# Optimization experiments

Measured on AMD Instinct MI355X. Metric: run time of the kernel, lower is better.

Reference implementation:

```python
import jax, jax.numpy as jnp
import numpy as np

NF = 64          # num_features
DG = 8           # deform_groups (== weight groups == offset groups)
KK = 9           # 3x3 kernel taps
OFF_CH = DG * 2 * KK   # 144 offset channels
MSK_CH = DG * KK       # 72 mask channels


def conv3x3(x, w):
    # x: [B,C,H,W], w: [O,I,3,3], stride 1, pad 1, no bias
    return jax.lax.conv_general_dilated(
        x, w, window_strides=(1, 1), padding=((1, 1), (1, 1)),
        dimension_numbers=('NCHW', 'OIHW', 'NCHW'))


def deform_conv(x, offset, mask, w, b):
    """Modulated deformable conv (torchvision DeformConv2d semantics).
    x: [B,C,H,W]; offset: [B,2*DG*KK,H,W] (per group/tap (dy,dx) pairs);
    mask: [B,DG*KK,H,W] (already sigmoid'ed); w: [C, C//DG, 3, 3]; b: [C].
    """
    B, C, H, W = x.shape
    Cg = C // DG
    off = offset.reshape(B, DG, KK, 2, H, W)
    dy, dx = off[:, :, :, 0], off[:, :, :, 1]          # [B,G,K,H,W]
    ky = (jnp.arange(KK) // 3 - 1).astype(x.dtype).reshape(1, 1, KK, 1, 1)
    kx = (jnp.arange(KK) % 3 - 1).astype(x.dtype).reshape(1, 1, KK, 1, 1)
    py = dy + ky + jnp.arange(H, dtype=x.dtype).reshape(1, 1, 1, H, 1)
    px = dx + kx + jnp.arange(W, dtype=x.dtype).reshape(1, 1, 1, 1, W)

    xf = x.reshape(B, DG, Cg, H * W)
    y0 = jnp.floor(py)
    x0 = jnp.floor(px)
    ly = py - y0
    lx = px - x0

    acc = jnp.zeros((B, DG, Cg, KK * H * W), dtype=x.dtype)
    for yy, wy in ((y0, 1.0 - ly), (y0 + 1.0, ly)):
        for xx, wx in ((x0, 1.0 - lx), (x0 + 1.0, lx)):
            valid = (yy >= 0) & (yy < H) & (xx >= 0) & (xx < W)
            yi = jnp.clip(yy, 0, H - 1).astype(jnp.int32)
            xi = jnp.clip(xx, 0, W - 1).astype(jnp.int32)
            idx = (yi * W + xi).reshape(B, DG, KK * H * W)
            v = jnp.take_along_axis(xf, idx[:, :, None, :], axis=3)  # [B,G,Cg,KHW]
            wgt = jnp.where(valid, wy * wx, 0.0).reshape(B, DG, 1, KK * H * W)
            acc = acc + v * wgt

    sampled = acc.reshape(B, DG, Cg, KK, H * W)
    sampled = sampled * mask.reshape(B, DG, 1, KK, H * W)
    wg = w.reshape(DG, C // DG, Cg, KK)                 # [G, Og, Cg, K]
    out = jnp.einsum('gock,bgckn->bgon', wg, sampled)   # [B,G,Og,HW]
    return out.reshape(B, C, H, W) + b.reshape(1, C, 1, 1)


def offset_gen(o):
    # chunk into 3 along channels: offset = cat(o1,o2) = first 144 ch, mask = sigmoid(last 72)
    return o[:, :OFF_CH], jax.nn.sigmoid(o[:, OFF_CH:])


def setup_inputs() -> dict:
    key = jax.random.key(0)
    ks = jax.random.split(key, 16)
    s = 0.05
    inp = {
        'burst_feat': jax.random.normal(ks[0], (1, 8, NF, 96, 96), jnp.float32),
        'bottleneck_w': jax.random.normal(ks[1], (NF, 2 * NF, 3, 3), jnp.float32) * s,
    }
    for i in range(4):
        inp[f'off_w{i+1}'] = jax.random.normal(ks[2 + i], (OFF_CH + MSK_CH, NF, 3, 3), jnp.float32) * s
        inp[f'def_w{i+1}'] = jax.random.normal(ks[6 + i], (NF, NF // DG, 3, 3), jnp.float32) * s
        inp[f'def_b{i+1}'] = jax.random.normal(ks[10 + i], (NF,), jnp.float32) * s
    return inp


def reference(burst_feat, bottleneck_w,
              off_w1, off_w2, off_w3, off_w4,
              def_w1, def_w2, def_w3, def_w4,
              def_b1, def_b2, def_b3, def_b4):
    B, N, F, H, W = burst_feat.shape
    ref = jnp.broadcast_to(burst_feat[:, 0:1], (B, N, F, H, W))
    feat = jnp.concatenate([burst_feat, ref], axis=2).reshape(B * N, 2 * F, H, W)
    feat = conv3x3(feat, bottleneck_w)
    for ow, dw, db in ((off_w1, def_w1, def_b1), (off_w2, def_w2, def_b2),
                       (off_w3, def_w3, def_b3), (off_w4, def_w4, def_b4)):
        offset, mask = offset_gen(conv3x3(feat, ow))
        feat = deform_conv(feat, offset, mask, dw, db)
    return feat.reshape(B, N, F, H, W)
```

## Files before the change

### kernel.cpp

```cpp
#include <hip/hip_runtime.h>
#include <math.h>

#define HW    9216
#define HDIM  96
#define WDIM  96
#define NIMG  8
#define CF    64
#define OFFCH 144
#define MSKCH 72
#define OMC   216
#define NT    36
#define LSTR  44

typedef unsigned short u16;
typedef unsigned int   u32;
typedef _Float16 f16;
typedef __attribute__((ext_vector_type(8))) _Float16 f16x8;
typedef __attribute__((ext_vector_type(4))) float f32x4;
typedef __attribute__((ext_vector_type(4))) u32 u32x4;

__device__ inline u16 f16b(f16 h){ u16 r; __builtin_memcpy(&r, &h, 2); return r; }
__device__ inline f16 b16f(u16 b){ f16 h; __builtin_memcpy(&h, &b, 2); return h; }

__global__ void pack_w_k(const float* __restrict__ bw,
                         const float* __restrict__ ow0, const float* __restrict__ ow1,
                         const float* __restrict__ ow2, const float* __restrict__ ow3,
                         const float* __restrict__ dw0, const float* __restrict__ dw1,
                         const float* __restrict__ dw2, const float* __restrict__ dw3,
                         u16* __restrict__ wp, float* __restrict__ dwp)
{
    const float* ows[4] = {ow0, ow1, ow2, ow3};
    const float* dws[4] = {dw0, dw1, dw2, dw3};
    int total = 73728 + 4 * 124416;
    for (int j = blockIdx.x * blockDim.x + threadIdx.x; j < total;
         j += gridDim.x * blockDim.x) {
        if (j < 73728) {
            int oc = j / 1152, r = j % 1152, ci = r / 9, tap = r % 9;
            wp[(size_t)(oc * 9 + tap) * 128 + ci] = f16b((f16)bw[j]);
        } else {
            int k = j - 73728;
            int layer = k / 124416, r = k % 124416;
            int oc = r / 576, r3 = r % 576, ci = r3 / 9, tap = r3 % 9;
            wp[73728 + (size_t)layer * 129024 + (size_t)(oc * 9 + tap) * 64 + ci] =
                f16b((f16)ows[layer][r]);
        }
    }
    for (int j = blockIdx.x * blockDim.x + threadIdx.x; j < 4 * 4608;
         j += gridDim.x * blockDim.x) {
        int layer = j / 4608, e = j % 4608;
        wp[73728 + (size_t)layer * 129024 + 124416 + e] = 0;
    }
    for (int j = blockIdx.x * blockDim.x + threadIdx.x; j < 4 * 8 * 576;
         j += gridDim.x * blockDim.x) {
        int layer = j / 4608, r = j % 4608, g = r / 576, e = r % 576;
        int kk = e / 64, c = (e / 8) % 8, o = e % 8;
        dwp[j] = dws[layer][(size_t)(g * 8 + o) * 72 + c * 9 + kk];
    }
}

__global__ __launch_bounds__(256) void prep_cat_k(
    const float* __restrict__ burst, u16* __restrict__ cat)
{
    __shared__ float tb[32 * 257];
    const int id = blockIdx.x;
    const int n = id & 7, tile = id >> 3;
    const int oy = (tile / 6) * 16, ox = (tile % 6) * 16;
    const int tid = threadIdx.x;

    for (int pass = 0; pass < 4; ++pass) {
        const float* src = (pass < 2) ? burst + (size_t)n * CF * HW : burst;
        const int chb = (pass & 1) * 32;
        __syncthreads();
        {
            int c = tid >> 3, q = tid & 7;
            const float* sp = src + (size_t)(chb + c) * HW;
#pragma unroll
            for (int rr = 0; rr < 2; ++rr) {
                int row = q * 2 + rr;
                const float* rp = sp + (oy + row) * WDIM + ox;
#pragma unroll
                for (int jj = 0; jj < 4; ++jj) {
                    f32x4 v = *(const f32x4*)(rp + jj * 4);
                    int px = row * 16 + jj * 4;
                    tb[c * 257 + px + 0] = v.x;
                    tb[c * 257 + px + 1] = v.y;
                    tb[c * 257 + px + 2] = v.z;
                    tb[c * 257 + px + 3] = v.w;
                }
            }
        }
        __syncthreads();
        {
            int p = tid;
#pragma unroll
            for (int cq = 0; cq < 4; ++cq) {
                u32 wd[4];
#pragma unroll
                for (int e = 0; e < 4; ++e) {
                    int c0 = cq * 8 + e * 2;
                    u16 h0 = f16b((f16)tb[c0 * 257 + p]);
                    u16 h1 = f16b((f16)tb[(c0 + 1) * 257 + p]);
                    wd[e] = (u32)h0 | ((u32)h1 << 16);
                }
                u32x4 hv = {wd[0], wd[1], wd[2], wd[3]};
                int plane = pass * 4 + cq;
                *(u32x4*)(cat + ((size_t)((n * NT + tile) * 16 + plane) * 256 + p) * 8) = hv;
            }
        }
    }
}

template<int PLANES, int MODE>
__global__ __launch_bounds__(256, 4) void conv_mfma_k(
    const u16* __restrict__ inb,
    const u16* __restrict__ w_hi,
    u16* __restrict__ om_out,
    u16* __restrict__ out_feat)
{
    __shared__ __align__(16) u16 lds[324 * LSTR];

    const int CIN = PLANES * 8;
    const int id = blockIdx.x;
    const int n = id & 7, w = id >> 3;
    const int tile = (MODE == 0) ? (w >> 1) : (w / 7);
    const int ocg  = (MODE == 0) ? (w & 1)  : (w % 7);
    const int tid = threadIdx.x;
    const int wv = tid >> 6, lane = tid & 63;
    const int lx = lane & 15, lg = lane >> 4;
    const int oy = (tile / 6) * 16, ox = (tile % 6) * 16;

    f32x4 acc1[2][4];
#pragma unroll
    for (int t = 0; t < 2; ++t)
#pragma unroll
        for (int r = 0; r < 4; ++r)
            acc1[t][r] = (f32x4){0.f, 0.f, 0.f, 0.f};

    const u16* inb_n = inb + (size_t)(n * NT) * PLANES * 2048;
    const u16* wr0 = w_hi + (size_t)((ocg * 32 + lx) * 9) * CIN + lg * 8;
    const u16* wr1 = w_hi + (size_t)((ocg * 32 + 16 + lx) * 9) * CIN + lg * 8;

    for (int chk = 0; chk < PLANES / 4; ++chk) {
        __syncthreads();
        for (int u = tid; u < 1296; u += 256) {
            int pos = u >> 2, q = u & 3;
            int yy = pos / 18, xx = pos - yy * 18;
            int gy = oy + yy - 1, gx = ox + xx - 1;
            u32x4 val = {0u, 0u, 0u, 0u};
            if (gy >= 0 && gy < HDIM && gx >= 0 && gx < WDIM) {
                int tof = (gy >> 4) * 6 + (gx >> 4);
                int pin = (gy & 15) * 16 + (gx & 15);
                val = *(const u32x4*)(inb_n +
                    ((size_t)(tof * PLANES + chk * 4 + q) * 256 + pin) * 8);
            }
            *(u32x4*)(lds + pos * LSTR + q * 8) = val;
        }
        __syncthreads();

        const u16* wc0 = wr0 + chk * 32;
        const u16* wc1 = wr1 + chk * 32;
        const u16* lbase = lds + (wv * 4) * 18 * LSTR + lx * LSTR + lg * 8;

        f16x8 aw0 = *(const f16x8*)(wc0);
        f16x8 aw1 = *(const f16x8*)(wc1);
        f16x8 bfr[4];
#pragma unroll
        for (int r = 0; r < 4; ++r)
            bfr[r] = *(const f16x8*)(lbase + r * 18 * LSTR);

#pragma unroll
        for (int tap = 0; tap < 9; ++tap) {
            f16x8 na0, na1, nb[4];
            if (tap < 8) {
                const int ntap = tap + 1;
                const int nky = ntap / 3, nkx = ntap - nky * 3;
                na0 = *(const f16x8*)(wc0 + (size_t)ntap * CIN);
                na1 = *(const f16x8*)(wc1 + (size_t)ntap * CIN);
#pragma unroll
                for (int r = 0; r < 4; ++r)
                    nb[r] = *(const f16x8*)(lbase + ((r + nky) * 18 + nkx) * LSTR);
            }
#pragma unroll
            for (int r = 0; r < 4; ++r) {
                acc1[0][r] = __builtin_amdgcn_mfma_f32_16x16x32_f16(aw0, bfr[r], acc1[0][r], 0, 0, 0);
                acc1[1][r] = __builtin_amdgcn_mfma_f32_16x16x32_f16(aw1, bfr[r], acc1[1][r], 0, 0, 0);
            }
            if (tap < 8) {
                aw0 = na0; aw1 = na1;
#pragma unroll
                for (int r = 0; r < 4; ++r) bfr[r] = nb[r];
            }
        }
    }

    if (MODE == 0) {
        __syncthreads();
        u16* tb = lds;
#pragma unroll
        for (int t = 0; t < 2; ++t)
#pragma unroll
            for (int r = 0; r < 4; ++r) {
                int px = (wv * 4 + r) * 16 + lx;
#pragma unroll
                for (int v = 0; v < 4; ++v)
                    tb[px * LSTR + t * 16 + lg * 4 + v] = f16b((f16)acc1[t][r][v]);
            }
        __syncthreads();
        const int p = tid;
        const u16* srcr = tb + p * LSTR;
#pragma unroll
        for (int cq = 0; cq < 4; ++cq) {
            *(u32x4*)(out_feat + ((size_t)((n * NT + tile) * 8 + ocg * 4 + cq) * 256 + p) * 8)
                = *(const u32x4*)(srcr + cq * 8);
        }
    } else {
        __syncthreads();
        u16* tb = lds;
#pragma unroll
        for (int t = 0; t < 2; ++t) {
            const bool sig = (ocg * 32 + t * 16) >= OFFCH;
#pragma unroll
            for (int r = 0; r < 4; ++r) {
                int px = (wv * 4 + r) * 16 + lx;
#pragma unroll
                for (int v = 0; v < 4; ++v) {
                    float val = acc1[t][r][v];
                    if (sig) val = 1.f / (1.f + __expf(-val));
                    tb[(t * 16 + lg * 4 + v) * 264 + px] = f16b((f16)val);
                }
            }
        }
        __syncthreads();
        const int ocl = tid >> 3, q = tid & 7;
        const int ch = ocg * 32 + ocl;
        if (ch < OMC) {
            u16* dst = om_out + ((size_t)(n * NT + tile) * OMC + ch) * 256;
            const u16* srcr = tb + ocl * 264;
#pragma unroll
            for (int j = 0; j < 4; ++j) {
                int un = (q + j * 8) * 8;
                *(u32x4*)(dst + un) = *(const u32x4*)(srcr + un);
            }
        }
    }
}

template<int LAST>
__global__ __launch_bounds__(256, 4) void deform_k(
    const u16* __restrict__ feat,
    const u16* __restrict__ om,
    const float* __restrict__ wgtp, const float* __restrict__ bias,
    u16* __restrict__ out_feat, float* __restrict__ out32)
{
    const int id = blockIdx.x;
    const int n = id & 7, w = id >> 3;
    const int tile = w >> 3, g = w & 7;

    const int ty = threadIdx.x >> 4, tx = threadIdx.x & 15;
    const int h  = (tile / 6) * 16 + ty;
    const int wx = (tile % 6) * 16 + tx;
    const int pix = h * WDIM + wx;
    const int pixT = ty * 16 + tx;

    const float* wg = wgtp + (size_t)g * 576;
    const u16* ob = om + (size_t)(n * NT + tile) * OMC * 256;
    const u16* fbase = feat + (size_t)(n * NT) * 8 * 2048 + g * 2048;

    float acc[8];
#pragma unroll
    for (int o = 0; o < 8; ++o) acc[o] = 0.f;

#pragma unroll
    for (int k = 0; k < 9; ++k) {
        float dy = (float)b16f(ob[(g * 18 + 2 * k    ) * 256 + pixT]);
        float dx = (float)b16f(ob[(g * 18 + 2 * k + 1) * 256 + pixT]);
        float m  = (float)b16f(ob[(OFFCH + g * 9 + k) * 256 + pixT]);

        float py = dy + (float)(k / 3 - 1) + (float)h;
        float px = dx + (float)(k % 3 - 1) + (float)wx;
        float y0f = floorf(py), x0f = floorf(px);
        float ly = py - y0f, lx = px - x0f;
        int y0 = (int)y0f, x0 = (int)x0f;
        int y1 = y0 + 1,   x1 = x0 + 1;

        bool vy0 = (y0 >= 0) && (y0 < HDIM);
        bool vy1 = (y1 >= 0) && (y1 < HDIM);
        bool vx0 = (x0 >= 0) && (x0 < WDIM);
        bool vx1 = (x1 >= 0) && (x1 < WDIM);

        float w00 = (vy0 && vx0) ? (1.f - ly) * (1.f - lx) : 0.f;
        float w01 = (vy0 && vx1) ? (1.f - ly) * lx         : 0.f;
        float w10 = (vy1 && vx0) ? ly * (1.f - lx)         : 0.f;
        float w11 = (vy1 && vx1) ? ly * lx                 : 0.f;

        int y0c = min(max(y0, 0), HDIM - 1), y1c = min(max(y1, 0), HDIM - 1);
        int x0c = min(max(x0, 0), WDIM - 1), x1c = min(max(x1, 0), WDIM - 1);

        auto ga = [&](int y, int x) -> const f16x8* {
            int tof = (y >> 4) * 6 + (x >> 4);
            int pin = (y & 15) * 16 + (x & 15);
            return (const f16x8*)(fbase + (size_t)tof * 16384 + pin * 8);
        };
        f16x8 C00 = *ga(y0c, x0c);
        f16x8 C01 = *ga(y0c, x1c);
        f16x8 C10 = *ga(y1c, x0c);
        f16x8 C11 = *ga(y1c, x1c);

#pragma unroll
        for (int c = 0; c < 8; ++c) {
            float v =      w00 * (float)C00[c];
            v = fmaf(w01, (float)C01[c], v);
            v = fmaf(w10, (float)C10[c], v);
            v = fmaf(w11, (float)C11[c], v);
            v *= m;
            const float* w8 = wg + (k * 8 + c) * 8;
#pragma unroll
            for (int o = 0; o < 8; ++o)
                acc[o] = fmaf(w8[o], v, acc[o]);
        }
    }

    if (LAST) {
#pragma unroll
        for (int o = 0; o < 8; ++o)
            out32[((size_t)n * CF + g * 8 + o) * HW + pix] = acc[o] + bias[g * 8 + o];
    } else {
        u16 hb[8];
#pragma unroll
        for (int o = 0; o < 8; ++o)
            hb[o] = f16b((f16)(acc[o] + bias[g * 8 + o]));
        u32x4 hv;
        hv.x = (u32)hb[0] | ((u32)hb[1] << 16); hv.y = (u32)hb[2] | ((u32)hb[3] << 16);
        hv.z = (u32)hb[4] | ((u32)hb[5] << 16); hv.w = (u32)hb[6] | ((u32)hb[7] << 16);
        *(u32x4*)(out_feat + ((size_t)((n * NT + tile) * 8 + g) * 256 + pixT) * 8) = hv;
    }
}

extern "C" void kernel_launch(void* const* d_in, const int* in_sizes, int n_in,
                              void* d_out, int out_size, void* d_ws, size_t ws_size,
                              hipStream_t stream) {
    const float* burst = (const float*)d_in[0];
    const float* bw    = (const float*)d_in[1];

    const float* ow[4]; const float* dw[4]; const float* db[4];
    bool interleaved = (in_sizes[3] == 64 * 8 * 9);
    for (int i = 0; i < 4; ++i) {
        if (interleaved) {
            ow[i] = (const float*)d_in[2 + 3 * i];
            dw[i] = (const float*)d_in[3 + 3 * i];
            db[i] = (const float*)d_in[4 + 3 * i];
        } else {
            ow[i] = (const float*)d_in[2 + i];
            dw[i] = (const float*)d_in[6 + i];
            db[i] = (const float*)d_in[10 + i];
        }
    }

    float* out = (float*)d_out;

    u16*   om    = (u16*)d_ws;
    u16*   featB = om + 15925248;
    u16*   wp    = featB + 4718592;
    float* dwp   = (float*)(wp + 589824);
    u16*   cat   = (u16*)d_ws;
    u16*   featA = (u16*)d_out;

    const u16* wp_b = wp;
    const u16* wp_o[4];
    for (int i = 0; i < 4; ++i)
        wp_o[i] = wp + 73728 + (size_t)i * 129024;

    pack_w_k<<<dim3(512), dim3(256), 0, stream>>>(
        bw, ow[0], ow[1], ow[2], ow[3], dw[0], dw[1], dw[2], dw[3], wp, dwp);
    prep_cat_k<<<dim3(288), dim3(256), 0, stream>>>(burst, cat);

    conv_mfma_k<16, 0><<<dim3(576), dim3(256), 0, stream>>>(
        cat, wp_b, nullptr, featA);

    u16* fx = featA;
    u16* fy = featB;
    for (int i = 0; i < 4; ++i) {
        conv_mfma_k<8, 1><<<dim3(2016), dim3(256), 0, stream>>>(
            fx, wp_o[i], om, nullptr);
        if (i < 3) {
            deform_k<0><<<dim3(2304), dim3(256), 0, stream>>>(
                fx, om, dwp + (size_t)i * 4608, db[i], fy, nullptr);
            u16* t = fx; fx = fy; fy = t;
        } else {
            deform_k<1><<<dim3(2304), dim3(256), 0, stream>>>(
                fx, om, dwp + (size_t)i * 4608, db[i], nullptr, out);
        }
    }
}
```

Before: 385.5 us.

## Widen offset-conv tiles to 16x32 so each weight fragment feeds two pixel tiles

The offset/mask convolution kernel gains a TX template parameter. With TX=2 each block covers two horizontally adjacent 16x16 tiles: it stages a wider halo in LDS and reuses every weight fragment across both tiles, which halves the grid and the global weight loads. The cost is doubled accumulator registers and a larger LDS footprint, so launch bounds drop to 3 blocks per CU. The epilogue writes both tiles, and the LDS row stride changes to 40 for the wide path.

```diff
diff --git a/kernel.cpp b/kernel.cpp
--- a/kernel.cpp
+++ b/kernel.cpp
@@ -10,7 +10,6 @@
 #define MSKCH 72
 #define OMC   216
 #define NT    36
-#define LSTR  44
 
 typedef unsigned short u16;
 typedef unsigned int   u32;
@@ -110,31 +109,44 @@
     }
 }
 
-template<int PLANES, int MODE>
-__global__ __launch_bounds__(256, 4) void conv_mfma_k(
+template<int PLANES, int MODE, int TX>
+__global__ __launch_bounds__(256, 3) void conv_mfma_k(
     const u16* __restrict__ inb,
     const u16* __restrict__ w_hi,
     u16* __restrict__ om_out,
     u16* __restrict__ out_feat)
 {
-    __shared__ __align__(16) u16 lds[324 * LSTR];
-
-    const int CIN = PLANES * 8;
+    constexpr int CIN   = PLANES * 8;
+    constexpr int HALOW = 16 * TX + 2;
+    constexpr int HSTR  = (TX == 2) ? 40 : 44;
+    constexpr int POSN  = 18 * HALOW;
+    __shared__ __align__(16) u16 lds[POSN * HSTR];
+
     const int id = blockIdx.x;
     const int n = id & 7, w = id >> 3;
-    const int tile = (MODE == 0) ? (w >> 1) : (w / 7);
-    const int ocg  = (MODE == 0) ? (w & 1)  : (w % 7);
+    int tile0, ocg, oy, ox;
+    if (TX == 1) {
+        tile0 = (MODE == 0) ? (w >> 1) : (w / 7);
+        ocg   = (MODE == 0) ? (w & 1)  : (w % 7);
+        oy = (tile0 / 6) * 16; ox = (tile0 % 6) * 16;
+    } else {
+        int region = w / 7; ocg = w % 7;
+        int trow = region / 3, tp = region % 3;
+        tile0 = trow * 6 + tp * 2;
+        oy = trow * 16; ox = tp * 32;
+    }
     const int tid = threadIdx.x;
     const int wv = tid >> 6, lane = tid & 63;
     const int lx = lane & 15, lg = lane >> 4;
-    const int oy = (tile / 6) * 16, ox = (tile % 6) * 16;
-
-    f32x4 acc1[2][4];
+
+    f32x4 acc[2][4][TX];
 #pragma unroll
     for (int t = 0; t < 2; ++t)
 #pragma unroll
         for (int r = 0; r < 4; ++r)
-            acc1[t][r] = (f32x4){0.f, 0.f, 0.f, 0.f};
+#pragma unroll
+            for (int s = 0; s < TX; ++s)
+                acc[t][r][s] = (f32x4){0.f, 0.f, 0.f, 0.f};
 
     const u16* inb_n = inb + (size_t)(n * NT) * PLANES * 2048;
     const u16* wr0 = w_hi + (size_t)((ocg * 32 + lx) * 9) * CIN + lg * 8;
@@ -142,9 +154,9 @@
 
     for (int chk = 0; chk < PLANES / 4; ++chk) {
         __syncthreads();
-        for (int u = tid; u < 1296; u += 256) {
+        for (int u = tid; u < POSN * 4; u += 256) {
             int pos = u >> 2, q = u & 3;
-            int yy = pos / 18, xx = pos - yy * 18;
+            int yy = pos / HALOW, xx = pos - yy * HALOW;
             int gy = oy + yy - 1, gx = ox + xx - 1;
             u32x4 val = {0u, 0u, 0u, 0u};
             if (gy >= 0 && gy < HDIM && gx >= 0 && gx < WDIM) {
@@ -153,42 +165,70 @@
                 val = *(const u32x4*)(inb_n +
                     ((size_t)(tof * PLANES + chk * 4 + q) * 256 + pin) * 8);
             }
-            *(u32x4*)(lds + pos * LSTR + q * 8) = val;
+            *(u32x4*)(lds + pos * HSTR + q * 8) = val;
         }
         __syncthreads();
 
         const u16* wc0 = wr0 + chk * 32;
         const u16* wc1 = wr1 + chk * 32;
-        const u16* lbase = lds + (wv * 4) * 18 * LSTR + lx * LSTR + lg * 8;
-
-        f16x8 aw0 = *(const f16x8*)(wc0);
-        f16x8 aw1 = *(const f16x8*)(wc1);
-        f16x8 bfr[4];
-#pragma unroll
-        for (int r = 0; r < 4; ++r)
-            bfr[r] = *(const f16x8*)(lbase + r * 18 * LSTR);
-
-#pragma unroll
-        for (int tap = 0; tap < 9; ++tap) {
-            f16x8 na0, na1, nb[4];
-            if (tap < 8) {
-                const int ntap = tap + 1;
-                const int nky = ntap / 3, nkx = ntap - nky * 3;
-                na0 = *(const f16x8*)(wc0 + (size_t)ntap * CIN);
-                na1 = *(const f16x8*)(wc1 + (size_t)ntap * CIN);
+
+        if (TX == 1) {
+            const u16* lbase = lds + (wv * 4) * HALOW * HSTR + lx * HSTR + lg * 8;
+            f16x8 aw0 = *(const f16x8*)(wc0);
+            f16x8 aw1 = *(const f16x8*)(wc1);
+            f16x8 bfr[4];
+#pragma unroll
+            for (int r = 0; r < 4; ++r)
+                bfr[r] = *(const f16x8*)(lbase + r * HALOW * HSTR);
+#pragma unroll
+            for (int tap = 0; tap < 9; ++tap) {
+                f16x8 na0, na1, nb[4];
+                if (tap < 8) {
+                    const int ntap = tap + 1;
+                    const int nky = ntap / 3, nkx = ntap - nky * 3;
+                    na0 = *(const f16x8*)(wc0 + (size_t)ntap * CIN);
+                    na1 = *(const f16x8*)(wc1 + (size_t)ntap * CIN);
+#pragma unroll
+                    for (int r = 0; r < 4; ++r)
+                        nb[r] = *(const f16x8*)(lbase + ((r + nky) * HALOW + nkx) * HSTR);
+                }
+#pragma unroll
+                for (int r = 0; r < 4; ++r) {
+                    acc[0][r][0] = __builtin_amdgcn_mfma_f32_16x16x32_f16(aw0, bfr[r], acc[0][r][0], 0, 0, 0);
+                    acc[1][r][0] = __builtin_amdgcn_mfma_f32_16x16x32_f16(aw1, bfr[r], acc[1][r][0], 0, 0, 0);
+                }
+                if (tap < 8) {
+                    aw0 = na0; aw1 = na1;
+#pragma unroll
+                    for (int r = 0; r < 4; ++r) bfr[r] = nb[r];
+                }
+            }
+        } else {
+            f16x8 aw0 = *(const f16x8*)(wc0);
+            f16x8 aw1 = *(const f16x8*)(wc1);
+#pragma unroll
+            for (int tap = 0; tap < 9; ++tap) {
+                f16x8 na0, na1;
+                if (tap < 8) {
+                    na0 = *(const f16x8*)(wc0 + (size_t)(tap + 1) * CIN);
+                    na1 = *(const f16x8*)(wc1 + (size_t)(tap + 1) * CIN);
+                }
+                const int ky = tap / 3, kx = tap - ky * 3;
+                f16x8 bfr[4][2];
 #pragma unroll
                 for (int r = 0; r < 4; ++r)
-                    nb[r] = *(const f16x8*)(lbase + ((r + nky) * 18 + nkx) * LSTR);
-            }
-#pragma unroll
-            for (int r = 0; r < 4; ++r) {
-                acc1[0][r] = __builtin_amdgcn_mfma_f32_16x16x32_f16(aw0, bfr[r], acc1[0][r], 0, 0, 0);
-                acc1[1][r] = __builtin_amdgcn_mfma_f32_16x16x32_f16(aw1, bfr[r], acc1[1][r], 0, 0, 0);
-            }
-            if (tap < 8) {
-                aw0 = na0; aw1 = na1;
-#pragma unroll
-                for (int r = 0; r < 4; ++r) bfr[r] = nb[r];
+#pragma unroll
+                    for (int s = 0; s < 2; ++s)
+                        bfr[r][s] = *(const f16x8*)(lds +
+                            ((size_t)((wv * 4 + r + ky) * HALOW + s * 16 + lx + kx)) * HSTR + lg * 8);
+#pragma unroll
+                for (int r = 0; r < 4; ++r)
+#pragma unroll
+                    for (int s = 0; s < 2; ++s) {
+                        acc[0][r][s] = __builtin_amdgcn_mfma_f32_16x16x32_f16(aw0, bfr[r][s], acc[0][r][s], 0, 0, 0);
+                        acc[1][r][s] = __builtin_amdgcn_mfma_f32_16x16x32_f16(aw1, bfr[r][s], acc[1][r][s], 0, 0, 0);
+                    }
+                if (tap < 8) { aw0 = na0; aw1 = na1; }
             }
         }
     }
@@ -203,14 +243,14 @@
                 int px = (wv * 4 + r) * 16 + lx;
 #pragma unroll
                 for (int v = 0; v < 4; ++v)
-                    tb[px * LSTR + t * 16 + lg * 4 + v] = f16b((f16)acc1[t][r][v]);
+                    tb[px * HSTR + t * 16 + lg * 4 + v] = f16b((f16)acc[t][r][0][v]);
             }
         __syncthreads();
         const int p = tid;
-        const u16* srcr = tb + p * LSTR;
+        const u16* srcr = tb + p * HSTR;
 #pragma unroll
         for (int cq = 0; cq < 4; ++cq) {
-            *(u32x4*)(out_feat + ((size_t)((n * NT + tile) * 8 + ocg * 4 + cq) * 256 + p) * 8)
+            *(u32x4*)(out_feat + ((size_t)((n * NT + tile0) * 8 + ocg * 4 + cq) * 256 + p) * 8)
                 = *(const u32x4*)(srcr + cq * 8);
         }
     } else {
@@ -221,25 +261,30 @@
             const bool sig = (ocg * 32 + t * 16) >= OFFCH;
 #pragma unroll
             for (int r = 0; r < 4; ++r) {
-                int px = (wv * 4 + r) * 16 + lx;
-#pragma unroll
-                for (int v = 0; v < 4; ++v) {
-                    float val = acc1[t][r][v];
-                    if (sig) val = 1.f / (1.f + __expf(-val));
-                    tb[(t * 16 + lg * 4 + v) * 264 + px] = f16b((f16)val);
-                }
+                int rowpx = (wv * 4 + r) * 16 + lx;
+#pragma unroll
+                for (int s = 0; s < 2; ++s)
+#pragma unroll
+                    for (int v = 0; v < 4; ++v) {
+                        float val = acc[t][r][s][v];
+                        if (sig) val = 1.f / (1.f + __expf(-val));
+                        tb[(t * 16 + lg * 4 + v) * 514 + s * 256 + rowpx] = f16b((f16)val);
+                    }
             }
         }
         __syncthreads();
         const int ocl = tid >> 3, q = tid & 7;
         const int ch = ocg * 32 + ocl;
         if (ch < OMC) {
-            u16* dst = om_out + ((size_t)(n * NT + tile) * OMC + ch) * 256;
-            const u16* srcr = tb + ocl * 264;
-#pragma unroll
-            for (int j = 0; j < 4; ++j) {
-                int un = (q + j * 8) * 8;
-                *(u32x4*)(dst + un) = *(const u32x4*)(srcr + un);
+            const u16* srcr = tb + ocl * 514;
+#pragma unroll
+            for (int s = 0; s < 2; ++s) {
+                u16* dst = om_out + ((size_t)(n * NT + tile0 + s) * OMC + ch) * 256;
+#pragma unroll
+                for (int j = 0; j < 4; ++j) {
+                    int un = (q + j * 8) * 8;
+                    *(u32x4*)(dst + un) = *(const u32x4*)(srcr + s * 256 + un);
+                }
             }
         }
     }
@@ -374,13 +419,13 @@
         bw, ow[0], ow[1], ow[2], ow[3], dw[0], dw[1], dw[2], dw[3], wp, dwp);
     prep_cat_k<<<dim3(288), dim3(256), 0, stream>>>(burst, cat);
 
-    conv_mfma_k<16, 0><<<dim3(576), dim3(256), 0, stream>>>(
+    conv_mfma_k<16, 0, 1><<<dim3(576), dim3(256), 0, stream>>>(
         cat, wp_b, nullptr, featA);
 
     u16* fx = featA;
     u16* fy = featB;
     for (int i = 0; i < 4; ++i) {
-        conv_mfma_k<8, 1><<<dim3(2016), dim3(256), 0, stream>>>(
+        conv_mfma_k<8, 1, 2><<<dim3(1008), dim3(256), 0, stream>>>(
             fx, wp_o[i], om, nullptr);
         if (i < 3) {
             deform_k<0><<<dim3(2304), dim3(256), 0, stream>>>(
```

Result: no change. 387.9 us (+0.6%).

## Split conv tile across eight waves and load B fragments per tap

Applied to the files above, without the earlier changes.

The MFMA conv kernel now runs 512 threads (8 waves) per block. Each wave covers 2 row-blocks of the 16x16 tile instead of 4, which halves the per-wave accumulators. The B-fragment software prefetch is dropped in favour of loading LDS fragments at each tap, and the store epilogues are redistributed across the larger block. The aim is lower register pressure and more waves in flight to hide latency, at the cost of less per-wave reuse of the weight fragments and less LDS-load/MFMA overlap.

```diff
diff --git a/kernel.cpp b/kernel.cpp
--- a/kernel.cpp
+++ b/kernel.cpp
@@ -111,7 +111,7 @@
 }
 
 template<int PLANES, int MODE>
-__global__ __launch_bounds__(256, 4) void conv_mfma_k(
+__global__ __launch_bounds__(512, 6) void conv_mfma_k(
     const u16* __restrict__ inb,
     const u16* __restrict__ w_hi,
     u16* __restrict__ om_out,
@@ -129,12 +129,12 @@
     const int lx = lane & 15, lg = lane >> 4;
     const int oy = (tile / 6) * 16, ox = (tile % 6) * 16;
 
-    f32x4 acc1[2][4];
+    f32x4 acc[2][2];
 #pragma unroll
     for (int t = 0; t < 2; ++t)
 #pragma unroll
-        for (int r = 0; r < 4; ++r)
-            acc1[t][r] = (f32x4){0.f, 0.f, 0.f, 0.f};
+        for (int r = 0; r < 2; ++r)
+            acc[t][r] = (f32x4){0.f, 0.f, 0.f, 0.f};
 
     const u16* inb_n = inb + (size_t)(n * NT) * PLANES * 2048;
     const u16* wr0 = w_hi + (size_t)((ocg * 32 + lx) * 9) * CIN + lg * 8;
@@ -142,7 +142,7 @@
 
     for (int chk = 0; chk < PLANES / 4; ++chk) {
         __syncthreads();
-        for (int u = tid; u < 1296; u += 256) {
+        for (int u = tid; u < 1296; u += 512) {
             int pos = u >> 2, q = u & 3;
             int yy = pos / 18, xx = pos - yy * 18;
             int gy = oy + yy - 1, gx = ox + xx - 1;
@@ -159,37 +159,29 @@
 
         const u16* wc0 = wr0 + chk * 32;
         const u16* wc1 = wr1 + chk * 32;
-        const u16* lbase = lds + (wv * 4) * 18 * LSTR + lx * LSTR + lg * 8;
+        const u16* lbase = lds + (wv * 2) * 18 * LSTR + lx * LSTR + lg * 8;
 
         f16x8 aw0 = *(const f16x8*)(wc0);
         f16x8 aw1 = *(const f16x8*)(wc1);
-        f16x8 bfr[4];
-#pragma unroll
-        for (int r = 0; r < 4; ++r)
-            bfr[r] = *(const f16x8*)(lbase + r * 18 * LSTR);
 
 #pragma unroll
         for (int tap = 0; tap < 9; ++tap) {
-            f16x8 na0, na1, nb[4];
+            f16x8 na0, na1;
             if (tap < 8) {
-                const int ntap = tap + 1;
-                const int nky = ntap / 3, nkx = ntap - nky * 3;
-                na0 = *(const f16x8*)(wc0 + (size_t)ntap * CIN);
-                na1 = *(const f16x8*)(wc1 + (size_t)ntap * CIN);
-#pragma unroll
-                for (int r = 0; r < 4; ++r)
-                    nb[r] = *(const f16x8*)(lbase + ((r + nky) * 18 + nkx) * LSTR);
-            }
-#pragma unroll
-            for (int r = 0; r < 4; ++r) {
-                acc1[0][r] = __builtin_amdgcn_mfma_f32_16x16x32_f16(aw0, bfr[r], acc1[0][r], 0, 0, 0);
-                acc1[1][r] = __builtin_amdgcn_mfma_f32_16x16x32_f16(aw1, bfr[r], acc1[1][r], 0, 0, 0);
-            }
-            if (tap < 8) {
-                aw0 = na0; aw1 = na1;
-#pragma unroll
-                for (int r = 0; r < 4; ++r) bfr[r] = nb[r];
-            }
+                na0 = *(const f16x8*)(wc0 + (size_t)(tap + 1) * CIN);
+                na1 = *(const f16x8*)(wc1 + (size_t)(tap + 1) * CIN);
+            }
+            const int ky = tap / 3, kx = tap - ky * 3;
+            f16x8 bfr[2];
+#pragma unroll
+            for (int r = 0; r < 2; ++r)
+                bfr[r] = *(const f16x8*)(lbase + ((r + ky) * 18 + kx) * LSTR);
+#pragma unroll
+            for (int r = 0; r < 2; ++r) {
+                acc[0][r] = __builtin_amdgcn_mfma_f32_16x16x32_f16(aw0, bfr[r], acc[0][r], 0, 0, 0);
+                acc[1][r] = __builtin_amdgcn_mfma_f32_16x16x32_f16(aw1, bfr[r], acc[1][r], 0, 0, 0);
+            }
+            if (tap < 8) { aw0 = na0; aw1 = na1; }
         }
     }
 
@@ -199,17 +191,18 @@
 #pragma unroll
         for (int t = 0; t < 2; ++t)
 #pragma unroll
-            for (int r = 0; r < 4; ++r) {
-                int px = (wv * 4 + r) * 16 + lx;
+            for (int r = 0; r < 2; ++r) {
+                int px = (wv * 2 + r) * 16 + lx;
 #pragma unroll
                 for (int v = 0; v < 4; ++v)
-                    tb[px * LSTR + t * 16 + lg * 4 + v] = f16b((f16)acc1[t][r][v]);
-            }
-        __syncthreads();
-        const int p = tid;
+                    tb[px * LSTR + t * 16 + lg * 4 + v] = f16b((f16)acc[t][r][v]);
+            }
+        __syncthreads();
+        const int p = tid & 255, half = tid >> 8;
         const u16* srcr = tb + p * LSTR;
 #pragma unroll
-        for (int cq = 0; cq < 4; ++cq) {
+        for (int j = 0; j < 2; ++j) {
+            int cq = half * 2 + j;
             *(u32x4*)(out_feat + ((size_t)((n * NT + tile) * 8 + ocg * 4 + cq) * 256 + p) * 8)
                 = *(const u32x4*)(srcr + cq * 8);
         }
@@ -220,25 +213,25 @@
         for (int t = 0; t < 2; ++t) {
             const bool sig = (ocg * 32 + t * 16) >= OFFCH;
 #pragma unroll
-            for (int r = 0; r < 4; ++r) {
-                int px = (wv * 4 + r) * 16 + lx;
+            for (int r = 0; r < 2; ++r) {
+                int px = (wv * 2 + r) * 16 + lx;
 #pragma unroll
                 for (int v = 0; v < 4; ++v) {
-                    float val = acc1[t][r][v];
+                    float val = acc[t][r][v];
                     if (sig) val = 1.f / (1.f + __expf(-val));
                     tb[(t * 16 + lg * 4 + v) * 264 + px] = f16b((f16)val);
                 }
             }
         }
         __syncthreads();
-        const int ocl = tid >> 3, q = tid & 7;
-        const int ch = ocg * 32 + ocl;
+        const int row = tid >> 4, q = tid & 15;
+        const int ch = ocg * 32 + row;
         if (ch < OMC) {
             u16* dst = om_out + ((size_t)(n * NT + tile) * OMC + ch) * 256;
-            const u16* srcr = tb + ocl * 264;
-#pragma unroll
-            for (int j = 0; j < 4; ++j) {
-                int un = (q + j * 8) * 8;
+            const u16* srcr = tb + row * 264;
+#pragma unroll
+            for (int j = 0; j < 2; ++j) {
+                int un = (q + j * 16) * 8;
                 *(u32x4*)(dst + un) = *(const u32x4*)(srcr + un);
             }
         }
@@ -374,13 +367,13 @@
         bw, ow[0], ow[1], ow[2], ow[3], dw[0], dw[1], dw[2], dw[3], wp, dwp);
     prep_cat_k<<<dim3(288), dim3(256), 0, stream>>>(burst, cat);
 
-    conv_mfma_k<16, 0><<<dim3(576), dim3(256), 0, stream>>>(
+    conv_mfma_k<16, 0><<<dim3(576), dim3(512), 0, stream>>>(
         cat, wp_b, nullptr, featA);
 
     u16* fx = featA;
     u16* fy = featB;
     for (int i = 0; i < 4; ++i) {
-        conv_mfma_k<8, 1><<<dim3(2016), dim3(256), 0, stream>>>(
+        conv_mfma_k<8, 1><<<dim3(2016), dim3(512), 0, stream>>>(
             fx, wp_o[i], om, nullptr);
         if (i < 3) {
             deform_k<0><<<dim3(2304), dim3(256), 0, stream>>>(
```

Measured after the change: 500.1 us. 1.3x slower.
